# Kernel optimization log

Hardware: AMD Instinct MI355X
Metric: run time of the kernel (lower is better)

Reference implementation:

```python
import jax, jax.numpy as jnp
import numpy as np

B = 256
H = W = 14
HW = H * W
TS = 0.03  # sigmoid temperature
TC = 0.07  # contrastive temperature
TP_K = int(HW * 0.1)   # 19
TN_K = int(HW * 0.5)   # 98
EPS_NORM = 1e-12
EPS_PD = 1e-6  # torch F.pairwise_distance eps


def _l2norm(x, axis):
    n = jnp.sqrt(jnp.sum(x * x, axis=axis, keepdims=True))
    return x / jnp.maximum(n, EPS_NORM)


def _conv(x, w):
    return jax.lax.conv_general_dilated(
        x, w, window_strides=(1, 1), padding='SAME',
        dimension_numbers=('NCHW', 'OIHW', 'NCHW'))


def setup_inputs() -> dict:
    key = jax.random.key(0)
    ks = jax.random.split(key, 7)
    ev = jax.random.normal(ks[0], (B, 384, H, W), dtype=jnp.float32)
    ea = jax.random.normal(ks[1], (B, 2048), dtype=jnp.float32)
    masks = jax.random.randint(ks[2], (B, H, W), 0, 2).astype(jnp.int32)
    masks = masks.at[:, 0, 0].set(1)  # guarantee nonzero mask area
    W_fc1 = jax.random.normal(ks[3], (512, 2048), dtype=jnp.float32) * 0.02
    W_fc2 = jax.random.normal(ks[4], (512, 512), dtype=jnp.float32) * 0.02
    W_conv1 = jax.random.normal(ks[5], (512, 384, 3, 3), dtype=jnp.float32) * 0.02
    W_conv2 = jax.random.normal(ks[6], (512, 512, 3, 3), dtype=jnp.float32) * 0.02
    return {'ev': ev, 'ea': ea, 'masks': masks, 'W_fc1': W_fc1,
            'W_fc2': W_fc2, 'W_conv1': W_conv1, 'W_conv2': W_conv2}


def reference(ev, ea, masks, W_fc1, W_fc2, W_conv1, W_conv2):
    # Audio_Proj: fc2(relu(fc1(ea)))  -> (B, 512)
    fa = jnp.maximum(ea @ W_fc1.T, 0.0) @ W_fc2.T

    # Visual_Proj: conv2(relu(conv1(ev))) -> (B, 512, 14, 14)
    fv_map = _conv(jnp.maximum(_conv(ev, W_conv1), 0.0), W_conv2)
    fv_map_norm = _l2norm(fv_map, axis=1)

    # masked mean pooling over the Ncut mask -> indicator vector (B, 512)
    m = masks.astype(jnp.float32)
    ind_vec = jnp.sum(fv_map * m[:, None], axis=(2, 3)) / jnp.sum(m, axis=(1, 2))[:, None]
    ind_vec_norm = _l2norm(ind_vec, axis=1)

    # Sij[i, j, p] = <fv_map_norm[i, :, p], ind_vec_norm[j]>  -> (B, B, HW)
    Sij = jnp.einsum('ichw,jc->ijhw', fv_map_norm, ind_vec_norm).reshape(B, B, HW)

    # per-row topk thresholds (kth largest / kth smallest)
    pos_thr = jax.lax.top_k(Sij, TP_K)[0][..., -1:]           # (B, B, 1)
    neg_thr = -jax.lax.top_k(-Sij, TN_K)[0][..., -1:]         # (B, B, 1)

    m_p = jax.nn.sigmoid((Sij - pos_thr) / TS)
    m_n = 1.0 - jax.nn.sigmoid((Sij - neg_thr) / TS)

    SP = jnp.sum(Sij * m_p, axis=-1) / jnp.sum(m_p, axis=-1)  # (B, B)
    SN = jnp.sum(Sij * m_n, axis=-1) / jnp.sum(m_n, axis=-1)  # (B, B)

    logits1 = jnp.concatenate([SP, SN], axis=1) / TC          # (B, 2B)
    logits2 = jnp.concatenate([SP.T, SN.T], axis=1) / TC
    labels = jnp.arange(B)
    loss1 = -jnp.mean(jax.nn.log_softmax(logits1, axis=-1)[labels, labels])
    loss2 = -jnp.mean(jax.nn.log_softmax(logits2, axis=-1)[labels, labels])

    # squared pairwise distance between detached ind_vec and fa (torch eps in diff)
    diff = jax.lax.stop_gradient(ind_vec)[:, None, :] - fa[None, :, :] + EPS_PD
    dist_mat = jnp.sum(diff * diff, axis=-1)                  # (B, B)

    ivn_d = jax.lax.stop_gradient(ind_vec_norm)
    vv_logits = ivn_d @ ivn_d.T
    eye = jnp.eye(B, dtype=jnp.float32)
    w = -vv_logits * (1.0 - eye) + eye
    dist_mat = dist_mat * w

    mask_mat = eye - (1.0 - eye) / (B - 1)
    loss3 = jnp.mean(jnp.maximum(jnp.sum(dist_mat * mask_mat, axis=1) + 0.6, 0.0))
    loss4 = jnp.mean(jnp.maximum(jnp.sum(dist_mat * mask_mat, axis=0) + 0.6, 0.0))

    return ((loss1 + loss2) / 2.0, (loss3 + loss4) / 2.0)
```

## Files before the change

### kernel.cpp

```cpp
#include <hip/hip_runtime.h>
#include <stdint.h>


typedef __attribute__((ext_vector_type(8))) short bf16x8;
typedef __attribute__((ext_vector_type(4))) float f32x4;

__device__ __forceinline__ unsigned short f2bf(float x) {
  unsigned u = __float_as_uint(x);
  unsigned r = u + 0x7FFFu + ((u >> 16) & 1u);
  return (unsigned short)(r >> 16);
}
__device__ __forceinline__ float bf2f(unsigned short h) {
  return __uint_as_float(((unsigned)h) << 16);
}

typedef const __attribute__((address_space(1))) void* gptr1_t;
typedef __attribute__((address_space(3))) void* lptr3_t;
__device__ __forceinline__ void gload_lds16(const void* g, void* l) {
  __builtin_amdgcn_global_load_lds((gptr1_t)g, (lptr3_t)l, 16, 0, 0);
}

__device__ __forceinline__ float waveSum(float v) {
#pragma unroll
  for (int m = 1; m < 64; m <<= 1) v += __shfl_xor(v, m, 64);
  return v;
}
__device__ __forceinline__ float waveMax(float v) {
#pragma unroll
  for (int m = 1; m < 64; m <<= 1) v = fmaxf(v, __shfl_xor(v, m, 64));
  return v;
}
template <int NW>
__device__ __forceinline__ float blockSum(float v) {
  __shared__ float sh[NW];
  v = waveSum(v);
  int wv = threadIdx.x >> 6, ln = threadIdx.x & 63;
  if (ln == 0) sh[wv] = v;
  __syncthreads();
  float r = 0.f;
#pragma unroll
  for (int w = 0; w < NW; ++w) r += sh[w];
  __syncthreads();
  return r;
}
template <int NW>
__device__ __forceinline__ float blockMax(float v) {
  __shared__ float sh[NW];
  v = waveMax(v);
  int wv = threadIdx.x >> 6, ln = threadIdx.x & 63;
  if (ln == 0) sh[wv] = v;
  __syncthreads();
  float r = -3.4e38f;
#pragma unroll
  for (int w = 0; w < NW; ++w) r = fmaxf(r, sh[w]);
  __syncthreads();
  return r;
}

#define RA 65536

template <int KC, int EPI>
__global__ __launch_bounds__(256, 2) void convtap6_k(
    const unsigned short* __restrict__ A, const unsigned short* __restrict__ Bw,
    unsigned short* __restrict__ C) {
  __shared__ __align__(16) short Ah[256 * 72];
  const int tid = threadIdx.x;
  const int wave = tid >> 6, lane = tid & 63;
  const int wm = wave >> 1, wn = wave & 1;
  const int quad = lane >> 4, tq = lane & 15;
  const int img = blockIdx.x, n0 = blockIdx.y * 128;

  int pab[7];
  {
    const int dh = tq >> 3;
    int wq = wm * 8 + (tq & 7);
    if (wq == 0) wq = 8;
    else if (wq == 15) wq = 7;
#pragma unroll
    for (int mi = 0; mi < 7; ++mi) {
      int pr = (1 + 2 * mi + dh) * 16 + wq;
      pab[mi] = pr * 72 + quad * 8;
    }
  }
  const int gb = (n0 >> 4) + wn * 4;

  const char* Ab = (const char*)A;
  const int l16 = lane * 16;

  f32x4 acc[7][4];
#pragma unroll
  for (int mi = 0; mi < 7; ++mi)
#pragma unroll
    for (int ni = 0; ni < 4; ++ni) {
      f32x4 z = {0.f, 0.f, 0.f, 0.f};
      acc[mi][ni] = z;
    }

  auto stageA = [&](int kc) {
    size_t s0 = ((size_t)kc * RA + img * 256) * 144;
#pragma unroll
    for (int i = 0; i < 9; ++i) {
      int c = wave + i * 4;
      gload_lds16(Ab + s0 + (size_t)c * 1024 + l16, (char*)Ah + c * 1024);
    }
  };

  stageA(0);
  __syncthreads();

  const int NS = KC * 9;
#pragma unroll 1
  for (int s = 0; s < NS; ++s) {
    int kc = s / 9, t = s - kc * 9;
    const int b16 = (t * KC + kc) * 4096 + gb * 128 + lane;
    bf16x8 bw0[4];
#pragma unroll
    for (int ni = 0; ni < 4; ++ni)
      bw0[ni] = *(const bf16x8*)&Bw[(size_t)(b16 + ni * 128) * 8];
    const int aoff = (((t / 3) - 1) * 16 + (t % 3) - 1) * 72;
    bf16x8 af0[7];
#pragma unroll
    for (int mi = 0; mi < 7; ++mi)
      af0[mi] = *(const bf16x8*)&Ah[pab[mi] + aoff];
    bf16x8 bw1[4];
#pragma unroll
    for (int ni = 0; ni < 4; ++ni)
      bw1[ni] = *(const bf16x8*)&Bw[(size_t)(b16 + ni * 128 + 64) * 8];
#pragma unroll
    for (int mi = 0; mi < 7; ++mi)
#pragma unroll
      for (int ni = 0; ni < 4; ++ni)
        acc[mi][ni] = __builtin_amdgcn_mfma_f32_16x16x32_bf16(
            af0[mi], bw0[ni], acc[mi][ni], 0, 0, 0);
    bf16x8 af1[7];
#pragma unroll
    for (int mi = 0; mi < 7; ++mi)
      af1[mi] = *(const bf16x8*)&Ah[pab[mi] + aoff + 32];
#pragma unroll
    for (int mi = 0; mi < 7; ++mi)
#pragma unroll
      for (int ni = 0; ni < 4; ++ni)
        acc[mi][ni] = __builtin_amdgcn_mfma_f32_16x16x32_bf16(
            af1[mi], bw1[ni], acc[mi][ni], 0, 0, 0);
    if (t == 8 && kc + 1 < KC) {
      __syncthreads();
      stageA(kc + 1);
      __syncthreads();
    }
  }

#pragma unroll
  for (int mi = 0; mi < 7; ++mi) {
#pragma unroll
    for (int r = 0; r < 4; ++r) {
      int idx = quad * 4 + r;
      int wv = wm * 8 + (idx & 7);
      if (wv == 0 || wv == 15) continue;
      int hh = 1 + 2 * mi + (idx >> 3);
      if (EPI == 0) {
        int cell = img * 256 + hh * 16 + wv;
        int slice = (n0 >> 6) + wn;
        size_t ob = ((size_t)slice * RA + cell) * 72 + tq;
#pragma unroll
        for (int ni = 0; ni < 4; ++ni)
          C[ob + ni * 16] = f2bf(fmaxf(acc[mi][ni][r], 0.f));
      } else {
        int p = (hh - 1) * 14 + (wv - 1);
        size_t ob = (size_t)(img * 196 + p) * 512 + n0 + wn * 64 + tq;
#pragma unroll
        for (int ni = 0; ni < 4; ++ni)
          C[ob + ni * 16] = f2bf(acc[mi][ni][r]);
      }
    }
  }
}

template <int K, int NLD, int EPI>
__global__ __launch_bounds__(256, 2) void gemm1_k(
    const unsigned short* __restrict__ A, const unsigned short* __restrict__ Bw,
    void* __restrict__ C, const float* __restrict__ rs) {
  __shared__ short As[128 * 64];
  __shared__ short Bs[128 * 64];
  const int tid = threadIdx.x;
  const int wave = tid >> 6, lane = tid & 63;
  const int m0 = blockIdx.x * 128, n0 = blockIdx.y * 128;
  const int rr8 = lane >> 3, seg = lane & 7, gseg = seg ^ rr8;
  const int wm = wave >> 1, wn = wave & 1;
  const int quad = lane >> 4, tq = lane & 15;

  size_t asrc[4], bsrc[4];
#pragma unroll
  for (int i8 = 0; i8 < 4; ++i8) {
    int rloc = wave * 32 + i8 * 8 + rr8;
    asrc[i8] = (size_t)(m0 + rloc) * K + gseg * 8;
    bsrc[i8] = (size_t)(n0 + rloc) * K + gseg * 8;
  }

  f32x4 acc[4][4];
#pragma unroll
  for (int mi = 0; mi < 4; ++mi)
#pragma unroll
    for (int ni = 0; ni < 4; ++ni) {
      f32x4 z = {0.f, 0.f, 0.f, 0.f};
      acc[mi][ni] = z;
    }

#pragma unroll 1
  for (int kc2 = 0; kc2 < K / 64; ++kc2) {
    int kb = kc2 * 64;
    __syncthreads();
#pragma unroll
    for (int i8 = 0; i8 < 4; ++i8) {
      gload_lds16(A + asrc[i8] + kb, &As[(wave * 32 + i8 * 8) * 64]);
      gload_lds16(Bw + bsrc[i8] + kb, &Bs[(wave * 32 + i8 * 8) * 64]);
    }
    __syncthreads();
#pragma unroll
    for (int h = 0; h < 2; ++h) {
      bf16x8 af[4], bfr[4];
#pragma unroll
      for (int mi = 0; mi < 4; ++mi) {
        int row = wm * 64 + mi * 16 + tq;
        af[mi] = *(const bf16x8*)&As[row * 64 +
                                     ((((h << 2) | quad) ^ (row & 7)) << 3)];
      }
#pragma unroll
      for (int ni = 0; ni < 4; ++ni) {
        int row = wn * 64 + ni * 16 + tq;
        bfr[ni] = *(const bf16x8*)&Bs[row * 64 +
                                      ((((h << 2) | quad) ^ (row & 7)) << 3)];
      }
#pragma unroll
      for (int mi = 0; mi < 4; ++mi)
#pragma unroll
        for (int ni = 0; ni < 4; ++ni)
          acc[mi][ni] = __builtin_amdgcn_mfma_f32_16x16x32_bf16(
              af[mi], bfr[ni], acc[mi][ni], 0, 0, 0);
    }
  }

#pragma unroll
  for (int mi = 0; mi < 4; ++mi) {
#pragma unroll
    for (int r = 0; r < 4; ++r) {
      int m = m0 + wm * 64 + mi * 16 + quad * 4 + r;
      float sc = (EPI == 3) ? rs[m] : 1.f;
      size_t obase = (size_t)m * NLD + n0 + wn * 64 + tq;
#pragma unroll
      for (int ni = 0; ni < 4; ++ni) {
        float v = acc[mi][ni][r];
        size_t idx = obase + ni * 16;
        if (EPI == 0)
          ((unsigned short*)C)[idx] = f2bf(fmaxf(v, 0.f));
        else if (EPI == 2)
          ((float*)C)[idx] = v;
        else
          ((float*)C)[idx] = v * sc;
      }
    }
  }
}

__global__ __launch_bounds__(256, 2) void gemm_xv_k(
    const unsigned short* __restrict__ ivpb, const unsigned short* __restrict__ fab,
    const unsigned short* __restrict__ indnb, float* __restrict__ Xm,
    float* __restrict__ Vm) {
  const unsigned short* A = blockIdx.z ? indnb : ivpb;
  const unsigned short* Bw = blockIdx.z ? indnb : fab;
  float* C = blockIdx.z ? Vm : Xm;
  __shared__ short As[128 * 64];
  __shared__ short Bs[128 * 64];
  const int tid = threadIdx.x;
  const int wave = tid >> 6, lane = tid & 63;
  const int m0 = blockIdx.x * 128, n0 = blockIdx.y * 128;
  const int rr8 = lane >> 3, seg = lane & 7, gseg = seg ^ rr8;
  const int wm = wave >> 1, wn = wave & 1;
  const int quad = lane >> 4, tq = lane & 15;
  size_t asrc[4], bsrc[4];
#pragma unroll
  for (int i8 = 0; i8 < 4; ++i8) {
    int rloc = wave * 32 + i8 * 8 + rr8;
    asrc[i8] = (size_t)(m0 + rloc) * 512 + gseg * 8;
    bsrc[i8] = (size_t)(n0 + rloc) * 512 + gseg * 8;
  }
  f32x4 acc[4][4];
#pragma unroll
  for (int mi = 0; mi < 4; ++mi)
#pragma unroll
    for (int ni = 0; ni < 4; ++ni) {
      f32x4 z = {0.f, 0.f, 0.f, 0.f};
      acc[mi][ni] = z;
    }
#pragma unroll 1
  for (int kc2 = 0; kc2 < 8; ++kc2) {
    int kb = kc2 * 64;
    __syncthreads();
#pragma unroll
    for (int i8 = 0; i8 < 4; ++i8) {
      gload_lds16(A + asrc[i8] + kb, &As[(wave * 32 + i8 * 8) * 64]);
      gload_lds16(Bw + bsrc[i8] + kb, &Bs[(wave * 32 + i8 * 8) * 64]);
    }
    __syncthreads();
#pragma unroll
    for (int h = 0; h < 2; ++h) {
      bf16x8 af[4], bfr[4];
#pragma unroll
      for (int mi = 0; mi < 4; ++mi) {
        int row = wm * 64 + mi * 16 + tq;
        af[mi] = *(const bf16x8*)&As[row * 64 +
                                     ((((h << 2) | quad) ^ (row & 7)) << 3)];
      }
#pragma unroll
      for (int ni = 0; ni < 4; ++ni) {
        int row = wn * 64 + ni * 16 + tq;
        bfr[ni] = *(const bf16x8*)&Bs[row * 64 +
                                      ((((h << 2) | quad) ^ (row & 7)) << 3)];
      }
#pragma unroll
      for (int mi = 0; mi < 4; ++mi)
#pragma unroll
        for (int ni = 0; ni < 4; ++ni)
          acc[mi][ni] = __builtin_amdgcn_mfma_f32_16x16x32_bf16(
              af[mi], bfr[ni], acc[mi][ni], 0, 0, 0);
    }
  }
#pragma unroll
  for (int mi = 0; mi < 4; ++mi)
#pragma unroll
    for (int r = 0; r < 4; ++r) {
      int m = m0 + wm * 64 + mi * 16 + quad * 4 + r;
      size_t obase = (size_t)m * 256 + n0 + wn * 64 + tq;
#pragma unroll
      for (int ni = 0; ni < 4; ++ni) C[obase + ni * 16] = acc[mi][ni][r];
    }
}

__global__ void prep_all_k(const float* __restrict__ ea,
                           const float* __restrict__ Wf1,
                           const float* __restrict__ Wf2,
                           const float* __restrict__ Wc1,
                           const float* __restrict__ Wc2,
                           unsigned short* __restrict__ eab,
                           unsigned short* __restrict__ wf1b,
                           unsigned short* __restrict__ wf2b,
                           unsigned short* __restrict__ wb1,
                           unsigned short* __restrict__ wb2,
                           unsigned int* __restrict__ x1u) {
  int i = blockIdx.x * 256 + threadIdx.x;
  if (i < 524288) {
    eab[i] = f2bf(ea[i]);
  } else if (i < 1572864) {
    int j = i - 524288;
    wf1b[j] = f2bf(Wf1[j]);
  } else if (i < 1835008) {
    int j = i - 1572864;
    wf2b[j] = f2bf(Wf2[j]);
  } else if (i < 3604480) {
    int j = i - 1835008;
    int t = j / (6 * 32768), r = j - t * (6 * 32768);
    int kc = r / 32768, r2 = r - kc * 32768;
    int g = r2 >> 10, h = (r2 >> 9) & 1, quad = (r2 >> 7) & 3;
    int tq = (r2 >> 3) & 15, jj = r2 & 7;
    int n = g * 16 + tq, cin = kc * 64 + h * 32 + quad * 8 + jj;
    wb1[j] = f2bf(Wc1[(n * 384 + cin) * 9 + t]);
  } else if (i < 5963776) {
    int j = i - 3604480;
    int t = j / (8 * 32768), r = j - t * (8 * 32768);
    int kc = r / 32768, r2 = r - kc * 32768;
    int g = r2 >> 10, h = (r2 >> 9) & 1, quad = (r2 >> 7) & 3;
    int tq = (r2 >> 3) & 15, jj = r2 & 7;
    int n = g * 16 + tq, cin = kc * 64 + h * 32 + quad * 8 + jj;
    wb2[j] = f2bf(Wc2[(n * 512 + cin) * 9 + t]);
  } else {
    int j = i - 5963776;
    int hr = j >> 8, u = j & 255;
    int slice = u >> 5, uu = u & 31;
    int b = hr / 60, c = hr - b * 60;
    int cell;
    if (c < 16) cell = c;
    else if (c < 32) cell = 240 + (c - 16);
    else if (c < 46) cell = (c - 31) * 16;
    else cell = (c - 45) * 16 + 15;
    x1u[((size_t)slice * RA + b * 256 + cell) * 36 + uu] = 0u;
  }
}

__global__ __launch_bounds__(256) void evpad_k(const float* __restrict__ ev,
                                               unsigned short* __restrict__ out) {
  int b = blockIdx.x, ct = blockIdx.y;
  __shared__ float tile[64][197];
  int tid = threadIdx.x;
  const float* src = ev + ((size_t)b * 384 + ct * 64) * 196;
#pragma unroll 1
  for (int it = 0; it < 49; ++it) {
    int idx = it * 256 + tid;
    int c = idx / 196, p = idx - c * 196;
    tile[c][p] = src[idx];
  }
  __syncthreads();
  unsigned short* dst = out + ((size_t)ct * RA + b * 256) * 72;
#pragma unroll 1
  for (int it = 0; it < 64; ++it) {
    int idx = it * 256 + tid;
    int cell = idx >> 6, c = idx & 63;
    int h = (cell >> 4) - 1, w = (cell & 15) - 1;
    float v = ((unsigned)h < 14u && (unsigned)w < 14u) ? tile[c][h * 14 + w]
                                                       : 0.f;
    dst[(size_t)cell * 72 + c] = f2bf(v);
  }
}


__global__ __launch_bounds__(512) void pool_k(
    const unsigned short* __restrict__ fv, const int* __restrict__ masks,
    unsigned short* __restrict__ indnb, unsigned short* __restrict__ ivpb,
    float* __restrict__ Pi, float* __restrict__ rn) {
  int b = blockIdx.x;
  int w = threadIdx.x >> 6, lane = threadIdx.x & 63;
  __shared__ float red[8][512];
  __shared__ float msh[8];
  float acc[8] = {0.f, 0.f, 0.f, 0.f, 0.f, 0.f, 0.f, 0.f};
  float msum = 0.f;
  for (int p = w; p < 196; p += 8) {
    float m = (float)masks[b * 196 + p];
    msum += m;
    uint4 d = *(const uint4*)(fv + (size_t)(b * 196 + p) * 512 + lane * 8);
    const unsigned short* hp = (const unsigned short*)&d;
    float ss = 0.f;
#pragma unroll
    for (int k = 0; k < 8; ++k) {
      float x = bf2f(hp[k]);
      ss += x * x;
      acc[k] += m * x;
    }
    ss = waveSum(ss);
    if (lane == 0) rn[b * 196 + p] = 1.f / fmaxf(sqrtf(ss), 1e-12f);
  }
#pragma unroll
  for (int k = 0; k < 8; ++k) red[w][lane * 8 + k] = acc[k];
  if (lane == 0) msh[w] = msum;
  __syncthreads();
  int tid = threadIdx.x;
  float s = 0.f, mtot = 0.f;
#pragma unroll
  for (int ww = 0; ww < 8; ++ww) {
    s += red[ww][tid];
    mtot += msh[ww];
  }
  float v = s / mtot;
  float ss2 = blockSum<8>(v * v);
  float sc = 1.f / fmaxf(sqrtf(ss2), 1e-12f);
  indnb[b * 512 + tid] = f2bf(v * sc);
  float ve = v + 1e-6f;
  ivpb[b * 512 + tid] = f2bf(ve);
  float p2 = blockSum<8>(ve * ve);
  if (tid == 0) Pi[b] = p2;
}

__global__ __launch_bounds__(512) void fanorm_k(const float* __restrict__ fa,
                                                unsigned short* __restrict__ fab,
                                                float* __restrict__ Qj) {
  int b = blockIdx.x, tid = threadIdx.x;
  float v = fa[b * 512 + tid];
  fab[b * 512 + tid] = f2bf(v);
  float q = blockSum<8>(v * v);
  if (tid == 0) Qj[b] = q;
}


__device__ __forceinline__ float radix_kth(unsigned k0, unsigned k1, unsigned k2,
                                           unsigned k3, int k) {
  unsigned prefix = 0;
  int kk = k;
#pragma unroll 1
  for (int bit = 31; bit >= 14; --bit) {
    unsigned thi = (prefix >> bit) | 1u;
    int c = __popcll(__ballot((k0 >> bit) == thi)) +
            __popcll(__ballot((k1 >> bit) == thi)) +
            __popcll(__ballot((k2 >> bit) == thi)) +
            __popcll(__ballot((k3 >> bit) == thi));
    if (kk <= c)
      prefix |= (1u << bit);
    else
      kk -= c;
  }
  unsigned u = (prefix & 0x80000000u) ? (prefix ^ 0x80000000u) : ~prefix;
  return __uint_as_float(u);
}
__device__ __forceinline__ unsigned sortkey(float x) {
  unsigned u = __float_as_uint(x);
  return u ^ (((int)u >> 31) | 0x80000000u);
}

__global__ __launch_bounds__(256) void spsn_k(const float* __restrict__ Sij,
                                              float* __restrict__ SP,
                                              float* __restrict__ SN) {
  int i = blockIdx.x, jg = blockIdx.y;
  int tid = threadIdx.x, wave = tid >> 6, lane = tid & 63;
  __shared__ float tile[196 * 65];
#pragma unroll 1
  for (int it = 0; it < 49; ++it) {
    int lin = it * 256 + tid;
    int p = lin >> 6, j = lin & 63;
    tile[p * 65 + j] = Sij[(size_t)(i * 196 + p) * 256 + jg * 64 + j];
  }
  __syncthreads();
#pragma unroll 1
  for (int jj = 0; jj < 16; ++jj) {
    int j = jj * 4 + wave;
    float v0 = tile[lane * 65 + j];
    float v1 = tile[(lane + 64) * 65 + j];
    float v2 = tile[(lane + 128) * 65 + j];
    bool val3 = lane < 4;
    float v3 = val3 ? tile[(lane + 192) * 65 + j] : 0.f;
    unsigned k0 = sortkey(v0), k1 = sortkey(v1), k2 = sortkey(v2);
    unsigned k3 = val3 ? sortkey(v3) : 0u;
    float thrP = radix_kth(k0, k1, k2, k3, 19);
    float thrN = radix_kth(k0, k1, k2, k3, 99);
    float spn = 0.f, spd = 0.f, snn = 0.f, snd = 0.f;
    const float invTS = 1.f / 0.03f;
#pragma unroll
    for (int q = 0; q < 4; ++q) {
      float v = (q == 0) ? v0 : (q == 1) ? v1 : (q == 2) ? v2 : v3;
      bool ok = (q < 3) || val3;
      if (ok) {
        float mp = 1.f / (1.f + __expf((thrP - v) * invTS));
        float mn = 1.f / (1.f + __expf((v - thrN) * invTS));
        spn += v * mp;
        spd += mp;
        snn += v * mn;
        snd += mn;
      }
    }
    spn = waveSum(spn); spd = waveSum(spd);
    snn = waveSum(snn); snd = waveSum(snd);
    if (lane == 0) {
      SP[i * 256 + jg * 64 + j] = spn / spd;
      SN[i * 256 + jg * 64 + j] = snn / snd;
    }
  }
}

__global__ __launch_bounds__(256) void loss12_k(const float* __restrict__ SP,
                                                const float* __restrict__ SN,
                                                float* __restrict__ out) {
  int r = blockIdx.x;
  int i = r & 255;
  bool col = r >= 256;
  int tid = threadIdx.x;
  const float invTC = 1.f / 0.07f;
  float a = (col ? SP[tid * 256 + i] : SP[i * 256 + tid]) * invTC;
  float b = (col ? SN[tid * 256 + i] : SN[i * 256 + tid]) * invTC;
  float mx = blockMax<4>(fmaxf(a, b));
  float se = blockSum<4>(__expf(a - mx) + __expf(b - mx));
  float lse = mx + __logf(se);
  if (tid == 0) {
    float diag = SP[i * 256 + i] * invTC;
    atomicAdd(out, -(diag - lse) * (1.f / 512.f));
  }
}

__global__ __launch_bounds__(256) void distcomb_k(
    const float* __restrict__ Pi, const float* __restrict__ Qj,
    const float* __restrict__ X, const float* __restrict__ V,
    float* __restrict__ val, float* __restrict__ out) {
  int i = blockIdx.x, j = threadIdx.x;
  float d = Pi[i] - 2.f * X[i * 256 + j] + Qj[j];
  float w = (i == j) ? 1.f : -V[i * 256 + j];
  float x = d * w;
  val[i * 256 + j] = x;
  __shared__ float diag_sh;
  if (j == i) diag_sh = x;
  float tot = blockSum<4>(x);
  if (j == 0) {
    float rs = diag_sh - (tot - diag_sh) * (1.f / 255.f);
    atomicAdd(out + 1, fmaxf(rs + 0.6f, 0.f) * (1.f / 512.f));
  }
}

__global__ __launch_bounds__(256) void loss4_k(const float* __restrict__ val,
                                               float* __restrict__ out) {
  int j = blockIdx.x, i = threadIdx.x;
  float x = val[i * 256 + j];
  __shared__ float diag_sh;
  if (i == j) diag_sh = x;
  float tot = blockSum<4>(x);
  if (i == 0) {
    float cs = diag_sh - (tot - diag_sh) * (1.f / 255.f);
    atomicAdd(out + 1, fmaxf(cs + 0.6f, 0.f) * (1.f / 512.f));
  }
}


extern "C" void kernel_launch(void* const* d_in, const int* in_sizes, int n_in,
                              void* d_out, int out_size, void* d_ws,
                              size_t ws_size, hipStream_t stream) {
  (void)in_sizes; (void)n_in; (void)out_size; (void)ws_size;
  const float* ev = (const float*)d_in[0];
  const float* ea = (const float*)d_in[1];
  const int* msk = (const int*)d_in[2];
  const float* Wf1 = (const float*)d_in[3];
  const float* Wf2 = (const float*)d_in[4];
  const float* Wc1 = (const float*)d_in[5];
  const float* Wc2 = (const float*)d_in[6];
  float* out = (float*)d_out;
  char* ws = (char*)d_ws;

  size_t off = 0;
  auto alloc = [&](size_t bytes) {
    void* p = ws + off;
    off = (off + bytes + 255) & ~(size_t)255;
    return p;
  };
  unsigned short* evb = (unsigned short*)alloc((size_t)6 * RA * 144);
  unsigned short* fv = evb;
  unsigned short* x1b = (unsigned short*)alloc((size_t)8 * RA * 144);
  float* Sij = (float*)x1b;
  unsigned short* wb1 = (unsigned short*)alloc((size_t)9 * 6 * 32768 * 2);
  unsigned short* wb2 = (unsigned short*)alloc((size_t)9 * 8 * 32768 * 2);
  unsigned short* eab = (unsigned short*)alloc((size_t)256 * 2048 * 2);
  unsigned short* wf1b = (unsigned short*)alloc((size_t)512 * 2048 * 2);
  unsigned short* wf2b = (unsigned short*)alloc((size_t)512 * 512 * 2);
  unsigned short* hb = (unsigned short*)alloc((size_t)256 * 512 * 2);
  float* fa = (float*)alloc((size_t)256 * 512 * 4);
  unsigned short* indnb = (unsigned short*)alloc((size_t)256 * 512 * 2);
  unsigned short* ivpb = (unsigned short*)alloc((size_t)256 * 512 * 2);
  unsigned short* fab = (unsigned short*)alloc((size_t)256 * 512 * 2);
  float* Pi = (float*)alloc(256 * 4);
  float* Qj = (float*)alloc(256 * 4);
  float* Xm = (float*)alloc((size_t)256 * 256 * 4);
  float* Vm = (float*)alloc((size_t)256 * 256 * 4);
  float* rn = (float*)alloc((size_t)50176 * 4);
  float* SP = (float*)alloc((size_t)256 * 256 * 4);
  float* SN = (float*)alloc((size_t)256 * 256 * 4);
  float* val = (float*)alloc((size_t)256 * 256 * 4);

  hipMemsetAsync(out, 0, 2 * sizeof(float), stream);

  prep_all_k<<<38656, 256, 0, stream>>>(ea, Wf1, Wf2, Wc1, Wc2, eab, wf1b,
                                        wf2b, wb1, wb2, (unsigned int*)x1b);
  evpad_k<<<dim3(256, 6), 256, 0, stream>>>(ev, evb);

  convtap6_k<6, 0><<<dim3(256, 4), 256, 0, stream>>>(evb, wb1, x1b);
  gemm1_k<2048, 512, 0><<<dim3(2, 4), 256, 0, stream>>>(eab, wf1b, hb, nullptr);
  gemm1_k<512, 512, 2><<<dim3(2, 4), 256, 0, stream>>>(hb, wf2b, fa, nullptr);
  convtap6_k<8, 1><<<dim3(256, 4), 256, 0, stream>>>(x1b, wb2, fv);

  pool_k<<<256, 512, 0, stream>>>(fv, msk, indnb, ivpb, Pi, rn);
  fanorm_k<<<256, 512, 0, stream>>>(fa, fab, Qj);

  gemm1_k<512, 256, 3><<<dim3(392, 2), 256, 0, stream>>>(fv, indnb, Sij, rn);
  gemm_xv_k<<<dim3(2, 2, 2), 256, 0, stream>>>(ivpb, fab, indnb, Xm, Vm);

  spsn_k<<<dim3(256, 4), 256, 0, stream>>>(Sij, SP, SN);
  loss12_k<<<512, 256, 0, stream>>>(SP, SN, out);
  distcomb_k<<<256, 256, 0, stream>>>(Pi, Qj, Xm, Vm, val, out);
  loss4_k<<<256, 256, 0, stream>>>(val, out);
}
```

Measured before the change: 840.3 us.

## Software-pipeline conv weight loads and fully unroll 3x3 tap loop

Restructures the implicit-GEMM conv main loop to fully unroll the nine filter taps per K chunk. It prefetches the next tap's B-weight fragments from global memory one step ahead, so their latency overlaps the current MFMA block. It precomputes LDS A offsets as byte addresses with compile-time tap offsets and raises wave priority around the MFMA sequence. This hides global load latency at the cost of extra registers, which may lower occupancy.

```diff
diff --git a/kernel.cpp b/kernel.cpp
--- a/kernel.cpp
+++ b/kernel.cpp
@@ -79,12 +79,13 @@
 #pragma unroll
     for (int mi = 0; mi < 7; ++mi) {
       int pr = (1 + 2 * mi + dh) * 16 + wq;
-      pab[mi] = pr * 72 + quad * 8;
+      pab[mi] = (pr - 17) * 144 + quad * 16;
     }
   }
   const int gb = (n0 >> 4) + wn * 4;
 
   const char* Ab = (const char*)A;
+  const char* AhB = (const char*)Ah;
   const int l16 = lane * 16;
 
   f32x4 acc[7][4];
@@ -106,43 +107,61 @@
   };
 
   stageA(0);
-  __syncthreads();
-
-  const int NS = KC * 9;
-#pragma unroll 1
-  for (int s = 0; s < NS; ++s) {
-    int kc = s / 9, t = s - kc * 9;
-    const int b16 = (t * KC + kc) * 4096 + gb * 128 + lane;
-    bf16x8 bw0[4];
+  bf16x8 b0[4], b1[4];
+  {
+    const size_t w0 = ((size_t)gb * 128 + lane) * 8;
 #pragma unroll
     for (int ni = 0; ni < 4; ++ni)
-      bw0[ni] = *(const bf16x8*)&Bw[(size_t)(b16 + ni * 128) * 8];
-    const int aoff = (((t / 3) - 1) * 16 + (t % 3) - 1) * 72;
-    bf16x8 af0[7];
-#pragma unroll
-    for (int mi = 0; mi < 7; ++mi)
-      af0[mi] = *(const bf16x8*)&Ah[pab[mi] + aoff];
-    bf16x8 bw1[4];
-#pragma unroll
-    for (int ni = 0; ni < 4; ++ni)
-      bw1[ni] = *(const bf16x8*)&Bw[(size_t)(b16 + ni * 128 + 64) * 8];
-#pragma unroll
-    for (int mi = 0; mi < 7; ++mi)
+      b0[ni] = *(const bf16x8*)&Bw[w0 + (size_t)ni * 1024];
+  }
+  __syncthreads();
+
+#pragma unroll 1
+  for (int kc = 0; kc < KC; ++kc) {
+    const size_t bk = ((size_t)kc * 4096 + gb * 128 + lane) * 8;
+#pragma unroll
+    for (int t = 0; t < 9; ++t) {
+      const size_t tof = (size_t)t * KC * 32768;
 #pragma unroll
       for (int ni = 0; ni < 4; ++ni)
-        acc[mi][ni] = __builtin_amdgcn_mfma_f32_16x16x32_bf16(
-            af0[mi], bw0[ni], acc[mi][ni], 0, 0, 0);
-    bf16x8 af1[7];
-#pragma unroll
-    for (int mi = 0; mi < 7; ++mi)
-      af1[mi] = *(const bf16x8*)&Ah[pab[mi] + aoff + 32];
-#pragma unroll
-    for (int mi = 0; mi < 7; ++mi)
-#pragma unroll
-      for (int ni = 0; ni < 4; ++ni)
-        acc[mi][ni] = __builtin_amdgcn_mfma_f32_16x16x32_bf16(
-            af1[mi], bw1[ni], acc[mi][ni], 0, 0, 0);
-    if (t == 8 && kc + 1 < KC) {
+        b1[ni] = *(const bf16x8*)&Bw[bk + tof + (size_t)ni * 1024 + 512];
+      bf16x8 b0n[4];
+      const bool last = (t == 8) && (kc == KC - 1);
+      if (!last) {
+        const size_t nbase =
+            (t < 8) ? bk + (size_t)(t + 1) * KC * 32768 : bk + 32768;
+#pragma unroll
+        for (int ni = 0; ni < 4; ++ni)
+          b0n[ni] = *(const bf16x8*)&Bw[nbase + (size_t)ni * 1024];
+      }
+      const int OFF = (17 + (t / 3 - 1) * 16 + (t % 3 - 1)) * 144;
+      bf16x8 af0[7], af1[7];
+#pragma unroll
+      for (int mi = 0; mi < 7; ++mi)
+        af0[mi] = *(const bf16x8*)(AhB + pab[mi] + OFF);
+#pragma unroll
+      for (int mi = 0; mi < 7; ++mi)
+        af1[mi] = *(const bf16x8*)(AhB + pab[mi] + OFF + 64);
+      __builtin_amdgcn_s_setprio(1);
+#pragma unroll
+      for (int mi = 0; mi < 7; ++mi)
+#pragma unroll
+        for (int ni = 0; ni < 4; ++ni)
+          acc[mi][ni] = __builtin_amdgcn_mfma_f32_16x16x32_bf16(
+              af0[mi], b0[ni], acc[mi][ni], 0, 0, 0);
+#pragma unroll
+      for (int mi = 0; mi < 7; ++mi)
+#pragma unroll
+        for (int ni = 0; ni < 4; ++ni)
+          acc[mi][ni] = __builtin_amdgcn_mfma_f32_16x16x32_bf16(
+              af1[mi], b1[ni], acc[mi][ni], 0, 0, 0);
+      __builtin_amdgcn_s_setprio(0);
+      if (!last) {
+#pragma unroll
+        for (int ni = 0; ni < 4; ++ni) b0[ni] = b0n[ni];
+      }
+    }
+    if (kc + 1 < KC) {
       __syncthreads();
       stageA(kc + 1);
       __syncthreads();
```

New measurement: 759.3 us. 9.6% less time.
